# Performance work log

Measured on AMD Instinct MI355X. Metric: run time of the kernel, lower is better.

Reference implementation:

```python
import jax, jax.numpy as jnp
import numpy as np

N_NODES = 100000
N_EDGES = 1600000
F_IN = 512
HID = 128
N_CLASS = 6


def setup_inputs() -> dict:
    key = jax.random.key(0)
    ks = jax.random.split(key, 12)
    def unif(k, shape, stdv):
        return jax.random.uniform(k, shape, jnp.float32, -stdv, stdv)
    s1 = 1.0 / np.sqrt(HID); s4 = 1.0 / np.sqrt(N_CLASS)
    return {
        "x": jax.random.normal(ks[0], (N_NODES, F_IN), jnp.float32),
        "edge_row": jax.random.randint(ks[1], (N_EDGES,), 0, N_NODES, jnp.int32),
        "edge_col": jax.random.randint(ks[2], (N_EDGES,), 0, N_NODES, jnp.int32),
        "edge_weight": jax.random.uniform(ks[3], (N_EDGES,), jnp.float32),
        "W1": unif(ks[4], (F_IN, HID), s1), "b1": unif(ks[5], (HID,), s1),
        "W2": unif(ks[6], (HID, HID), s1), "b2": unif(ks[7], (HID,), s1),
        "W3": unif(ks[8], (HID, HID), s1), "b3": unif(ks[9], (HID,), s1),
        "W4": unif(ks[10], (HID, N_CLASS), s4), "b4": unif(ks[11], (N_CLASS,), s4),
    }


def _gcn_layer(x, row, col, w_e, W, b):
    # support = x @ W  (dense mm), then spmm(adj, support) in COO form:
    # out[i] = sum_{(i,j) in E} A[i,j] * support[j]
    support = x @ W                              # [N, F_out]
    msgs = support[col] * w_e[:, None]           # [E, F_out] gather + scale
    agg = jax.ops.segment_sum(msgs, row, num_segments=N_NODES)
    return agg + b


def reference(x, edge_row, edge_col, edge_weight, W1, b1, W2, b2, W3, b3, W4, b4):
    # eval mode: F.dropout(training=False) is identity
    h = jax.nn.relu(_gcn_layer(x, edge_row, edge_col, edge_weight, W1, b1))
    h = jax.nn.relu(_gcn_layer(h, edge_row, edge_col, edge_weight, W2, b2))
    h = jax.nn.relu(_gcn_layer(h, edge_row, edge_col, edge_weight, W3, b3))
    return _gcn_layer(h, edge_row, edge_col, edge_weight, W4, b4)
```

## Files before the change

### kernel.cpp

```cpp
#include <hip/hip_runtime.h>
#include <cstdint>

constexpr int NN = 100000;
constexpr int NE = 1600000;
constexpr int FIN = 512;
constexpr int HID = 128;
constexpr int NCLS = 6;
constexpr int EPAD = NE + 3 * NN;

typedef __attribute__((ext_vector_type(8))) short short8v;
typedef __attribute__((ext_vector_type(4))) float f32x4;

constexpr float WINV = 1.0f / 32767.0f;

__device__ __forceinline__ unsigned short f2bf(float f) {
    uint32_t u = __float_as_uint(f);
    uint32_t r = u + 0x7FFFu + ((u >> 16) & 1u);
    return (unsigned short)(r >> 16);
}
__device__ __forceinline__ float bflo(uint32_t u) { return __uint_as_float(u << 16); }
__device__ __forceinline__ float bfhi(uint32_t u) { return __uint_as_float(u & 0xffff0000u); }

__device__ __forceinline__ void gl_lds16(const void* g, void* l) {
    __builtin_amdgcn_global_load_lds(
        (const __attribute__((address_space(1))) unsigned int*)(unsigned long long)g,
        (__attribute__((address_space(3))) unsigned int*)(unsigned int)(unsigned long long)l,
        16, 0, 0);
}

__device__ __forceinline__ void cvt_body(const float* __restrict__ W,
                                         unsigned short* __restrict__ Bp, int t) {
    const int lane = t & 63;
    const int fi = t >> 6;
    const int n = fi & 7, ks = fi >> 3;
    const int krow = ks * 32 + (lane >> 4) * 8;
    const int col = n * 16 + (lane & 15);
    short8v sv;
    #pragma unroll
    for (int j = 0; j < 8; ++j) sv[j] = (short)f2bf(W[(size_t)(krow + j) * HID + col]);
    *(short8v*)&Bp[(size_t)t * 8] = sv;
}

__global__ void cvt_w3(const float* __restrict__ W1, const float* __restrict__ W2,
                       const float* __restrict__ W3,
                       unsigned short* __restrict__ Bp1, unsigned short* __restrict__ Bp2,
                       unsigned short* __restrict__ Bp3) {
    const int t = blockIdx.x * blockDim.x + threadIdx.x;
    constexpr int T1 = (FIN / 32) * 8 * 64;
    constexpr int T2 = (HID / 32) * 8 * 64;
    if (t < T1)                cvt_body(W1, Bp1, t);
    else if (t < T1 + T2)      cvt_body(W2, Bp2, t - T1);
    else if (t < T1 + 2 * T2)  cvt_body(W3, Bp3, t - T1 - T2);
}

template<int K, bool ABF>
__launch_bounds__(320)
__global__ void gemm_lds(const void* __restrict__ Av, const unsigned short* __restrict__ Bp,
                         unsigned short* __restrict__ C) {
    constexpr int BM    = 160;
    constexpr int KS    = 32;
    constexpr int EB    = ABF ? 2 : 4;
    constexpr int ROWB  = KS * EB;
    constexpr int SLOTS = ROWB / 16;
    constexpr int SMSK  = SLOTS - 1;
    constexpr int CHUNK = BM * ROWB;
    constexpr int WBYT  = CHUNK / 5;
    constexpr int NISS  = WBYT / 1024;
    constexpr int NS    = K / KS;

    __shared__ __attribute__((aligned(16))) unsigned char lds[2 * CHUNK];

    const int tid  = threadIdx.x;
    const int lane = tid & 63;
    const int wave = tid >> 6;
    const int row0 = blockIdx.x * BM;
    const int lr   = lane & 15;
    const int kg   = lane >> 4;

    const unsigned char* Ab = (const unsigned char*)Av;
    const size_t rowbytes = (size_t)K * EB;

    auto stage = [&](int bufsel, int ks) {
        const size_t kbyte = (size_t)ks * ROWB;
        #pragma unroll
        for (int i = 0; i < NISS; ++i) {
            const int Lw   = wave * WBYT + i * 1024 + lane * 16;
            const int row  = Lw / ROWB;
            const int slot = (Lw >> 4) & SMSK;
            const int src  = slot ^ (row & SMSK);
            const unsigned char* g = Ab + (size_t)(row0 + row) * rowbytes + kbyte + src * 16;
            void* l = (void*)&lds[bufsel * CHUNK + wave * WBYT + i * 1024];
            gl_lds16(g, l);
        }
    };

    f32x4 acc[2][8] = {};

    stage(0, 0);

    int cur = 0;
    for (int ks = 0; ks < NS; ++ks) {
        short8v bfr[8];
        const unsigned short* bb = Bp + ((size_t)ks * 8 * 64 + lane) * 8;
        #pragma unroll
        for (int n = 0; n < 8; ++n)
            bfr[n] = *reinterpret_cast<const short8v*>(bb + (size_t)n * 64 * 8);

        if (ks + 1 < NS) {
            stage(cur ^ 1, ks + 1);
            asm volatile("s_waitcnt vmcnt(%0)" :: "i"(NISS) : "memory");
        } else {
            asm volatile("s_waitcnt vmcnt(0)" ::: "memory");
        }
        __builtin_amdgcn_sched_barrier(0);

        const unsigned char* base = &lds[cur * CHUNK];
        const int rA0 = wave * 32 + lr;
        const int rA1 = rA0 + 16;
        const int key = lr & SMSK;

        short8v a0, a1;
        if constexpr (ABF) {
            a0 = *(const short8v*)(base + rA0 * ROWB + ((kg ^ key) * 16));
            a1 = *(const short8v*)(base + rA1 * ROWB + ((kg ^ key) * 16));
        } else {
            const float4 f00 = *(const float4*)(base + rA0 * ROWB + (((2 * kg + 0) ^ key) * 16));
            const float4 f01 = *(const float4*)(base + rA0 * ROWB + (((2 * kg + 1) ^ key) * 16));
            const float4 f10 = *(const float4*)(base + rA1 * ROWB + (((2 * kg + 0) ^ key) * 16));
            const float4 f11 = *(const float4*)(base + rA1 * ROWB + (((2 * kg + 1) ^ key) * 16));
            a0[0] = (short)f2bf(f00.x); a0[1] = (short)f2bf(f00.y);
            a0[2] = (short)f2bf(f00.z); a0[3] = (short)f2bf(f00.w);
            a0[4] = (short)f2bf(f01.x); a0[5] = (short)f2bf(f01.y);
            a0[6] = (short)f2bf(f01.z); a0[7] = (short)f2bf(f01.w);
            a1[0] = (short)f2bf(f10.x); a1[1] = (short)f2bf(f10.y);
            a1[2] = (short)f2bf(f10.z); a1[3] = (short)f2bf(f10.w);
            a1[4] = (short)f2bf(f11.x); a1[5] = (short)f2bf(f11.y);
            a1[6] = (short)f2bf(f11.z); a1[7] = (short)f2bf(f11.w);
        }

        #pragma unroll
        for (int n = 0; n < 8; ++n) {
            acc[0][n] = __builtin_amdgcn_mfma_f32_16x16x32_bf16(a0, bfr[n], acc[0][n], 0, 0, 0);
            acc[1][n] = __builtin_amdgcn_mfma_f32_16x16x32_bf16(a1, bfr[n], acc[1][n], 0, 0, 0);
        }
        cur ^= 1;
    }

    #pragma unroll
    for (int m = 0; m < 2; ++m)
        #pragma unroll
        for (int n = 0; n < 8; ++n)
            #pragma unroll
            for (int i = 0; i < 4; ++i) {
                const int r = row0 + wave * 32 + m * 16 + kg * 4 + i;
                C[(size_t)r * HID + n * 16 + lr] = f2bf(acc[m][n][i]);
            }
}

__global__ void gemm_w4(const unsigned short* __restrict__ H, const float* __restrict__ W,
                        float* __restrict__ S, int M) {
    __shared__ float Ws[HID * NCLS];
    for (int i = threadIdx.x; i < HID * NCLS; i += blockDim.x) Ws[i] = W[i];
    __syncthreads();
    const int r = blockIdx.x * blockDim.x + threadIdx.x;
    if (r >= M) return;
    float acc[NCLS] = {};
    const unsigned short* h = &H[(size_t)r * HID];
    for (int k0 = 0; k0 < HID; k0 += 8) {
        const uint4 hv = *reinterpret_cast<const uint4*>(&h[k0]);
        float hf[8];
        hf[0] = bflo(hv.x); hf[1] = bfhi(hv.x);
        hf[2] = bflo(hv.y); hf[3] = bfhi(hv.y);
        hf[4] = bflo(hv.z); hf[5] = bfhi(hv.z);
        hf[6] = bflo(hv.w); hf[7] = bfhi(hv.w);
        #pragma unroll
        for (int u = 0; u < 8; ++u)
            #pragma unroll
            for (int j = 0; j < NCLS; ++j)
                acc[j] = fmaf(hf[u], Ws[(k0 + u) * NCLS + j], acc[j]);
    }
    #pragma unroll
    for (int j = 0; j < NCLS; ++j) S[(size_t)r * NCLS + j] = acc[j];
}

__global__ void hist_k(const int* __restrict__ erow, int* __restrict__ cnt) {
    const int e = blockIdx.x * blockDim.x + threadIdx.x;
    if (e < NE) atomicAdd(&cnt[erow[e]], 1);
}

__global__ void scan1_k(const int* __restrict__ in, int* __restrict__ out,
                        int* __restrict__ bsum, int n) {
    __shared__ int s[256];
    const int tid = threadIdx.x;
    const int gid = blockIdx.x * 256 + tid;
    const int v = (gid < NN) ? ((in[gid] + 3) & ~3) : 0;
    s[tid] = v;
    __syncthreads();
    for (int off = 1; off < 256; off <<= 1) {
        const int t = (tid >= off) ? s[tid - off] : 0;
        __syncthreads();
        s[tid] += t;
        __syncthreads();
    }
    if (gid < n) out[gid] = s[tid] - v;
    if (tid == 255) bsum[blockIdx.x] = s[255];
}

__global__ void scan2_k(int* __restrict__ bsum, int nb) {
    __shared__ int s[512];
    const int tid = threadIdx.x;
    const int v = (tid < nb) ? bsum[tid] : 0;
    s[tid] = v;
    __syncthreads();
    for (int off = 1; off < 512; off <<= 1) {
        const int t = (tid >= off) ? s[tid - off] : 0;
        __syncthreads();
        s[tid] += t;
        __syncthreads();
    }
    if (tid < nb) bsum[tid] = s[tid] - v;
}

__global__ void scan3_k(int* __restrict__ out, const int* __restrict__ bsum, int n) {
    const int gid = blockIdx.x * 256 + threadIdx.x;
    if (gid < n) out[gid] += bsum[blockIdx.x];
}

__global__ void scatter_k(const int* __restrict__ erow, const int* __restrict__ ecol,
                          const float* __restrict__ ew,
                          const int* __restrict__ row_ptr, int* __restrict__ cur,
                          uint32_t* __restrict__ edges) {
    const int e = blockIdx.x * blockDim.x + threadIdx.x;
    if (e >= NE) return;
    const int r = erow[e];
    const int pos = row_ptr[r] + atomicAdd(&cur[r], 1);
    const uint32_t wq = (uint32_t)(ew[e] * 32767.0f + 0.5f);
    edges[pos] = ((uint32_t)ecol[e] << 15) | wq;
}

__global__ void pad_k(const int* __restrict__ row_ptr, const int* __restrict__ cur,
                      uint32_t* __restrict__ edges) {
    const int r = blockIdx.x * blockDim.x + threadIdx.x;
    if (r >= NN) return;
    const int end = row_ptr[r + 1];
    for (int p = row_ptr[r] + cur[r]; p < end; ++p) edges[p] = 0u;
}

template<bool RELU>
__launch_bounds__(256)
__global__ void spmm_bf16(const int* __restrict__ row_ptr,
                          const uint32_t* __restrict__ edges,
                          const unsigned short* __restrict__ S,
                          const float* __restrict__ bias,
                          unsigned short* __restrict__ out) {
    const int lane = threadIdx.x & 63;
    const int row = blockIdx.x * 4 + (threadIdx.x >> 6);
    if (row >= NN) return;
    const int beg = row_ptr[row];
    const int end = row_ptr[row + 1];
    const int fo = lane * 2;
    float2 a0 = *reinterpret_cast<const float2*>(&bias[fo]);
    float2 a1 = {0.f, 0.f}, a2 = {0.f, 0.f}, a3 = {0.f, 0.f};

    int j = beg;
    for (; j + 16 <= end; j += 16) {
        uint4 e0 = *reinterpret_cast<const uint4*>(edges + j);
        uint4 e1 = *reinterpret_cast<const uint4*>(edges + j + 4);
        uint4 e2 = *reinterpret_cast<const uint4*>(edges + j + 8);
        uint4 e3 = *reinterpret_cast<const uint4*>(edges + j + 12);
        const uint32_t ea[16] = {e0.x, e0.y, e0.z, e0.w, e1.x, e1.y, e1.z, e1.w,
                                 e2.x, e2.y, e2.z, e2.w, e3.x, e3.y, e3.z, e3.w};
        uint32_t s[16];
        #pragma unroll
        for (int q = 0; q < 16; ++q)
            s[q] = *reinterpret_cast<const uint32_t*>(&S[(size_t)(ea[q] >> 15) * HID + fo]);
        #pragma unroll
        for (int q = 0; q < 4; ++q) {
            const float w0 = (float)(ea[q]      & 0x7FFFu) * WINV;
            const float w1 = (float)(ea[q + 4]  & 0x7FFFu) * WINV;
            const float w2 = (float)(ea[q + 8]  & 0x7FFFu) * WINV;
            const float w3 = (float)(ea[q + 12] & 0x7FFFu) * WINV;
            a0.x = fmaf(bflo(s[q]),      w0, a0.x); a0.y = fmaf(bfhi(s[q]),      w0, a0.y);
            a1.x = fmaf(bflo(s[q + 4]),  w1, a1.x); a1.y = fmaf(bfhi(s[q + 4]),  w1, a1.y);
            a2.x = fmaf(bflo(s[q + 8]),  w2, a2.x); a2.y = fmaf(bfhi(s[q + 8]),  w2, a2.y);
            a3.x = fmaf(bflo(s[q + 12]), w3, a3.x); a3.y = fmaf(bfhi(s[q + 12]), w3, a3.y);
        }
    }
    for (; j < end; j += 4) {
        const uint4 e = *reinterpret_cast<const uint4*>(edges + j);
        const uint32_t ea[4] = {e.x, e.y, e.z, e.w};
        uint32_t s[4];
        #pragma unroll
        for (int q = 0; q < 4; ++q)
            s[q] = *reinterpret_cast<const uint32_t*>(&S[(size_t)(ea[q] >> 15) * HID + fo]);
        const float w0 = (float)(ea[0] & 0x7FFFu) * WINV;
        const float w1 = (float)(ea[1] & 0x7FFFu) * WINV;
        const float w2 = (float)(ea[2] & 0x7FFFu) * WINV;
        const float w3 = (float)(ea[3] & 0x7FFFu) * WINV;
        a0.x = fmaf(bflo(s[0]), w0, a0.x); a0.y = fmaf(bfhi(s[0]), w0, a0.y);
        a1.x = fmaf(bflo(s[1]), w1, a1.x); a1.y = fmaf(bfhi(s[1]), w1, a1.y);
        a2.x = fmaf(bflo(s[2]), w2, a2.x); a2.y = fmaf(bfhi(s[2]), w2, a2.y);
        a3.x = fmaf(bflo(s[3]), w3, a3.x); a3.y = fmaf(bfhi(s[3]), w3, a3.y);
    }
    float fx = (a0.x + a1.x) + (a2.x + a3.x);
    float fy = (a0.y + a1.y) + (a2.y + a3.y);
    if (RELU) { fx = fmaxf(fx, 0.f); fy = fmaxf(fy, 0.f); }
    const uint32_t o = (uint32_t)f2bf(fx) | ((uint32_t)f2bf(fy) << 16);
    *reinterpret_cast<uint32_t*>(&out[(size_t)row * HID + fo]) = o;
}

__launch_bounds__(256)
__global__ void spmm6(const int* __restrict__ row_ptr,
                      const uint32_t* __restrict__ edges,
                      const float* __restrict__ S,
                      const float* __restrict__ bias,
                      float* __restrict__ out) {
    const int t = blockIdx.x * blockDim.x + threadIdx.x;
    const int row = t >> 4;
    const int sl = t & 15;
    if (row >= NN) return;
    const int beg = row_ptr[row];
    const int end = row_ptr[row + 1];
    float acc[NCLS] = {};
    for (int j = beg + sl; j < end; j += 16) {
        const uint32_t e = edges[j];
        const float w = (float)(e & 0x7FFFu) * WINV;
        const float* s = &S[(size_t)(e >> 15) * NCLS];
        #pragma unroll
        for (int k = 0; k < NCLS; ++k) acc[k] = fmaf(s[k], w, acc[k]);
    }
    #pragma unroll
    for (int off = 8; off > 0; off >>= 1)
        #pragma unroll
        for (int k = 0; k < NCLS; ++k) acc[k] += __shfl_xor(acc[k], off, 64);
    if (sl == 0) {
        #pragma unroll
        for (int k = 0; k < NCLS; ++k) out[(size_t)row * NCLS + k] = acc[k] + bias[k];
    }
}

extern "C" void kernel_launch(void* const* d_in, const int* in_sizes, int n_in,
                              void* d_out, int out_size, void* d_ws, size_t ws_size,
                              hipStream_t stream) {
    const float* x    = (const float*)d_in[0];
    const int*   erow = (const int*)d_in[1];
    const int*   ecol = (const int*)d_in[2];
    const float* ew   = (const float*)d_in[3];
    const float* W1 = (const float*)d_in[4];  const float* b1 = (const float*)d_in[5];
    const float* W2 = (const float*)d_in[6];  const float* b2 = (const float*)d_in[7];
    const float* W3 = (const float*)d_in[8];  const float* b3 = (const float*)d_in[9];
    const float* W4 = (const float*)d_in[10]; const float* b4 = (const float*)d_in[11];
    float* out = (float*)d_out;

    uint32_t*       edges_s = (uint32_t*)d_ws;
    unsigned short* sup16   = (unsigned short*)(edges_s + EPAD);
    unsigned short* h16     = sup16 + (size_t)NN * HID;
    float*          sup6    = (float*)(h16 + (size_t)NN * HID);
    unsigned short* Bp1     = (unsigned short*)(sup6 + (size_t)NN * NCLS);
    unsigned short* Bp2     = Bp1 + (size_t)FIN * HID;
    unsigned short* Bp3     = Bp2 + (size_t)HID * HID;
    int*            row_ptr = (int*)(Bp3 + (size_t)HID * HID);
    int*            row_cnt = row_ptr + (NN + 1);
    int*            row_cur = row_cnt + NN;
    int*            bsum    = row_cur + NN;

    const dim3 blk(256);
    const int  g_edge = (NE + 255) / 256;
    const int  NB = (NN + 1 + 255) / 256;

    cvt_w3<<<(12288 + 255) / 256, blk, 0, stream>>>(W1, W2, W3, Bp1, Bp2, Bp3);

    hipMemsetAsync(row_cnt, 0, (size_t)2 * NN * sizeof(int), stream);
    hist_k<<<g_edge, blk, 0, stream>>>(erow, row_cnt);
    scan1_k<<<NB, blk, 0, stream>>>(row_cnt, row_ptr, bsum, NN + 1);
    scan2_k<<<1, 512, 0, stream>>>(bsum, NB);
    scan3_k<<<NB, blk, 0, stream>>>(row_ptr, bsum, NN + 1);
    scatter_k<<<g_edge, blk, 0, stream>>>(erow, ecol, ew, row_ptr, row_cur, edges_s);
    pad_k<<<(NN + 255) / 256, blk, 0, stream>>>(row_ptr, row_cur, edges_s);

    const int g_gemm = NN / 160;
    const int g_spmm = NN / 4;

    gemm_lds<FIN, false><<<g_gemm, dim3(320), 0, stream>>>(x, Bp1, sup16);
    spmm_bf16<true><<<g_spmm, blk, 0, stream>>>(row_ptr, edges_s, sup16, b1, h16);
    gemm_lds<HID, true><<<g_gemm, dim3(320), 0, stream>>>(h16, Bp2, sup16);
    spmm_bf16<true><<<g_spmm, blk, 0, stream>>>(row_ptr, edges_s, sup16, b2, h16);
    gemm_lds<HID, true><<<g_gemm, dim3(320), 0, stream>>>(h16, Bp3, sup16);
    spmm_bf16<true><<<g_spmm, blk, 0, stream>>>(row_ptr, edges_s, sup16, b3, h16);
    gemm_w4<<<(NN + 255) / 256, blk, 0, stream>>>(h16, W4, sup6, NN);
    spmm6<<<(NN * 16 + 255) / 256, blk, 0, stream>>>(row_ptr, edges_s, sup6, b4, out);
}
```

Measured before the change: 449.6 us.

## Make bf16 SpMM persistent with software-prefetched row pointers and edges

```diff
diff --git a/kernel.cpp b/kernel.cpp
--- a/kernel.cpp
+++ b/kernel.cpp
@@ -252,61 +252,95 @@
                           const uint32_t* __restrict__ edges,
                           const unsigned short* __restrict__ S,
                           const float* __restrict__ bias,
-                          unsigned short* __restrict__ out) {
+                          unsigned short* __restrict__ out,
+                          int nwv) {
     const int lane = threadIdx.x & 63;
-    const int row = blockIdx.x * 4 + (threadIdx.x >> 6);
+    int row = (blockIdx.x * blockDim.x + threadIdx.x) >> 6;
     if (row >= NN) return;
-    const int beg = row_ptr[row];
-    const int end = row_ptr[row + 1];
     const int fo = lane * 2;
-    float2 a0 = *reinterpret_cast<const float2*>(&bias[fo]);
-    float2 a1 = {0.f, 0.f}, a2 = {0.f, 0.f}, a3 = {0.f, 0.f};
-
-    int j = beg;
-    for (; j + 16 <= end; j += 16) {
-        uint4 e0 = *reinterpret_cast<const uint4*>(edges + j);
-        uint4 e1 = *reinterpret_cast<const uint4*>(edges + j + 4);
-        uint4 e2 = *reinterpret_cast<const uint4*>(edges + j + 8);
-        uint4 e3 = *reinterpret_cast<const uint4*>(edges + j + 12);
-        const uint32_t ea[16] = {e0.x, e0.y, e0.z, e0.w, e1.x, e1.y, e1.z, e1.w,
-                                 e2.x, e2.y, e2.z, e2.w, e3.x, e3.y, e3.z, e3.w};
+    const float2 bv = *reinterpret_cast<const float2*>(&bias[fo]);
+
+    int beg = row_ptr[row];
+    int end = row_ptr[row + 1];
+    uint4 c0 = *reinterpret_cast<const uint4*>(edges + beg);
+    uint4 c1 = *reinterpret_cast<const uint4*>(edges + beg + 4);
+    uint4 c2 = *reinterpret_cast<const uint4*>(edges + beg + 8);
+    uint4 c3 = *reinterpret_cast<const uint4*>(edges + beg + 12);
+    int nrow = row + nwv;
+    int nbeg = 0, nend = 0;
+    if (nrow < NN) { nbeg = row_ptr[nrow]; nend = row_ptr[nrow + 1]; }
+
+    while (true) {
+        uint32_t ea[16] = {c0.x, c0.y, c0.z, c0.w, c1.x, c1.y, c1.z, c1.w,
+                           c2.x, c2.y, c2.z, c2.w, c3.x, c3.y, c3.z, c3.w};
         uint32_t s[16];
         #pragma unroll
         for (int q = 0; q < 16; ++q)
             s[q] = *reinterpret_cast<const uint32_t*>(&S[(size_t)(ea[q] >> 15) * HID + fo]);
-        #pragma unroll
-        for (int q = 0; q < 4; ++q) {
-            const float w0 = (float)(ea[q]      & 0x7FFFu) * WINV;
-            const float w1 = (float)(ea[q + 4]  & 0x7FFFu) * WINV;
-            const float w2 = (float)(ea[q + 8]  & 0x7FFFu) * WINV;
-            const float w3 = (float)(ea[q + 12] & 0x7FFFu) * WINV;
-            a0.x = fmaf(bflo(s[q]),      w0, a0.x); a0.y = fmaf(bfhi(s[q]),      w0, a0.y);
-            a1.x = fmaf(bflo(s[q + 4]),  w1, a1.x); a1.y = fmaf(bfhi(s[q + 4]),  w1, a1.y);
-            a2.x = fmaf(bflo(s[q + 8]),  w2, a2.x); a2.y = fmaf(bfhi(s[q + 8]),  w2, a2.y);
-            a3.x = fmaf(bflo(s[q + 12]), w3, a3.x); a3.y = fmaf(bfhi(s[q + 12]), w3, a3.y);
-        }
-    }
-    for (; j < end; j += 4) {
-        const uint4 e = *reinterpret_cast<const uint4*>(edges + j);
-        const uint32_t ea[4] = {e.x, e.y, e.z, e.w};
-        uint32_t s[4];
-        #pragma unroll
-        for (int q = 0; q < 4; ++q)
-            s[q] = *reinterpret_cast<const uint32_t*>(&S[(size_t)(ea[q] >> 15) * HID + fo]);
-        const float w0 = (float)(ea[0] & 0x7FFFu) * WINV;
-        const float w1 = (float)(ea[1] & 0x7FFFu) * WINV;
-        const float w2 = (float)(ea[2] & 0x7FFFu) * WINV;
-        const float w3 = (float)(ea[3] & 0x7FFFu) * WINV;
-        a0.x = fmaf(bflo(s[0]), w0, a0.x); a0.y = fmaf(bfhi(s[0]), w0, a0.y);
-        a1.x = fmaf(bflo(s[1]), w1, a1.x); a1.y = fmaf(bfhi(s[1]), w1, a1.y);
-        a2.x = fmaf(bflo(s[2]), w2, a2.x); a2.y = fmaf(bfhi(s[2]), w2, a2.y);
-        a3.x = fmaf(bflo(s[3]), w3, a3.x); a3.y = fmaf(bfhi(s[3]), w3, a3.y);
-    }
-    float fx = (a0.x + a1.x) + (a2.x + a3.x);
-    float fy = (a0.y + a1.y) + (a2.y + a3.y);
-    if (RELU) { fx = fmaxf(fx, 0.f); fy = fmaxf(fy, 0.f); }
-    const uint32_t o = (uint32_t)f2bf(fx) | ((uint32_t)f2bf(fy) << 16);
-    *reinterpret_cast<uint32_t*>(&out[(size_t)row * HID + fo]) = o;
+
+        uint4 n0, n1, n2, n3;
+        if (nrow < NN) {
+            n0 = *reinterpret_cast<const uint4*>(edges + nbeg);
+            n1 = *reinterpret_cast<const uint4*>(edges + nbeg + 4);
+            n2 = *reinterpret_cast<const uint4*>(edges + nbeg + 8);
+            n3 = *reinterpret_cast<const uint4*>(edges + nbeg + 12);
+        }
+        const int nnrow = nrow + nwv;
+        int nnbeg = 0, nnend = 0;
+        if (nnrow < NN) { nnbeg = row_ptr[nnrow]; nnend = row_ptr[nnrow + 1]; }
+
+        float2 a0 = bv, a1 = {0.f, 0.f}, a2 = {0.f, 0.f}, a3 = {0.f, 0.f};
+        if (beg < end) {
+            const float w0 = (float)(ea[0] & 0x7FFFu) * WINV;
+            const float w1 = (float)(ea[1] & 0x7FFFu) * WINV;
+            const float w2 = (float)(ea[2] & 0x7FFFu) * WINV;
+            const float w3 = (float)(ea[3] & 0x7FFFu) * WINV;
+            a0.x = fmaf(bflo(s[0]), w0, a0.x); a0.y = fmaf(bfhi(s[0]), w0, a0.y);
+            a1.x = fmaf(bflo(s[1]), w1, a1.x); a1.y = fmaf(bfhi(s[1]), w1, a1.y);
+            a2.x = fmaf(bflo(s[2]), w2, a2.x); a2.y = fmaf(bfhi(s[2]), w2, a2.y);
+            a3.x = fmaf(bflo(s[3]), w3, a3.x); a3.y = fmaf(bfhi(s[3]), w3, a3.y);
+        }
+        #pragma unroll
+        for (int g = 1; g < 4; ++g) {
+            if (beg + 4 * g < end) {
+                const float w0 = (float)(ea[4*g]     & 0x7FFFu) * WINV;
+                const float w1 = (float)(ea[4*g + 1] & 0x7FFFu) * WINV;
+                const float w2 = (float)(ea[4*g + 2] & 0x7FFFu) * WINV;
+                const float w3 = (float)(ea[4*g + 3] & 0x7FFFu) * WINV;
+                a0.x = fmaf(bflo(s[4*g]),     w0, a0.x); a0.y = fmaf(bfhi(s[4*g]),     w0, a0.y);
+                a1.x = fmaf(bflo(s[4*g + 1]), w1, a1.x); a1.y = fmaf(bfhi(s[4*g + 1]), w1, a1.y);
+                a2.x = fmaf(bflo(s[4*g + 2]), w2, a2.x); a2.y = fmaf(bfhi(s[4*g + 2]), w2, a2.y);
+                a3.x = fmaf(bflo(s[4*g + 3]), w3, a3.x); a3.y = fmaf(bfhi(s[4*g + 3]), w3, a3.y);
+            }
+        }
+        for (int j = beg + 16; j < end; j += 4) {
+            const uint4 e = *reinterpret_cast<const uint4*>(edges + j);
+            const uint32_t eb[4] = {e.x, e.y, e.z, e.w};
+            uint32_t t[4];
+            #pragma unroll
+            for (int q = 0; q < 4; ++q)
+                t[q] = *reinterpret_cast<const uint32_t*>(&S[(size_t)(eb[q] >> 15) * HID + fo]);
+            const float w0 = (float)(eb[0] & 0x7FFFu) * WINV;
+            const float w1 = (float)(eb[1] & 0x7FFFu) * WINV;
+            const float w2 = (float)(eb[2] & 0x7FFFu) * WINV;
+            const float w3 = (float)(eb[3] & 0x7FFFu) * WINV;
+            a0.x = fmaf(bflo(t[0]), w0, a0.x); a0.y = fmaf(bfhi(t[0]), w0, a0.y);
+            a1.x = fmaf(bflo(t[1]), w1, a1.x); a1.y = fmaf(bfhi(t[1]), w1, a1.y);
+            a2.x = fmaf(bflo(t[2]), w2, a2.x); a2.y = fmaf(bfhi(t[2]), w2, a2.y);
+            a3.x = fmaf(bflo(t[3]), w3, a3.x); a3.y = fmaf(bfhi(t[3]), w3, a3.y);
+        }
+
+        float fx = (a0.x + a1.x) + (a2.x + a3.x);
+        float fy = (a0.y + a1.y) + (a2.y + a3.y);
+        if (RELU) { fx = fmaxf(fx, 0.f); fy = fmaxf(fy, 0.f); }
+        const uint32_t o = (uint32_t)f2bf(fx) | ((uint32_t)f2bf(fy) << 16);
+        *reinterpret_cast<uint32_t*>(&out[(size_t)row * HID + fo]) = o;
+
+        if (nrow >= NN) break;
+        row = nrow; beg = nbeg; end = nend;
+        c0 = n0; c1 = n1; c2 = n2; c3 = n3;
+        nrow = nnrow; nbeg = nnbeg; nend = nnend;
+    }
 }
 
 __launch_bounds__(256)
@@ -379,14 +413,15 @@
     pad_k<<<(NN + 255) / 256, blk, 0, stream>>>(row_ptr, row_cur, edges_s);
 
     const int g_gemm = NN / 160;
-    const int g_spmm = NN / 4;
+    const int g_spmm = 1536;
+    const int nwv    = g_spmm * 4;
 
     gemm_lds<FIN, false><<<g_gemm, dim3(320), 0, stream>>>(x, Bp1, sup16);
-    spmm_bf16<true><<<g_spmm, blk, 0, stream>>>(row_ptr, edges_s, sup16, b1, h16);
+    spmm_bf16<true><<<g_spmm, blk, 0, stream>>>(row_ptr, edges_s, sup16, b1, h16, nwv);
     gemm_lds<HID, true><<<g_gemm, dim3(320), 0, stream>>>(h16, Bp2, sup16);
-    spmm_bf16<true><<<g_spmm, blk, 0, stream>>>(row_ptr, edges_s, sup16, b2, h16);
+    spmm_bf16<true><<<g_spmm, blk, 0, stream>>>(row_ptr, edges_s, sup16, b2, h16, nwv);
     gemm_lds<HID, true><<<g_gemm, dim3(320), 0, stream>>>(h16, Bp3, sup16);
-    spmm_bf16<true><<<g_spmm, blk, 0, stream>>>(row_ptr, edges_s, sup16, b3, h16);
+    spmm_bf16<true><<<g_spmm, blk, 0, stream>>>(row_ptr, edges_s, sup16, b3, h16, nwv);
     gemm_w4<<<(NN + 255) / 256, blk, 0, stream>>>(h16, W4, sup6, NN);
     spmm6<<<(NN * 16 + 255) / 256, blk, 0, stream>>>(row_ptr, edges_s, sup6, b4, out);
 }
```

After: 467.3 us. 3.9% more time.

## Split support matrix into 64-column halves and vectorize edge-preprocessing kernels

Applied to the files above, without the earlier changes.

```diff
diff --git a/kernel.cpp b/kernel.cpp
--- a/kernel.cpp
+++ b/kernel.cpp
@@ -56,7 +56,7 @@
 template<int K, bool ABF>
 __launch_bounds__(320)
 __global__ void gemm_lds(const void* __restrict__ Av, const unsigned short* __restrict__ Bp,
-                         unsigned short* __restrict__ C) {
+                         unsigned short* __restrict__ Sc) {
     constexpr int BM    = 160;
     constexpr int KS    = 32;
     constexpr int EB    = ABF ? 2 : 4;
@@ -153,7 +153,7 @@
             #pragma unroll
             for (int i = 0; i < 4; ++i) {
                 const int r = row0 + wave * 32 + m * 16 + kg * 4 + i;
-                C[(size_t)r * HID + n * 16 + lr] = f2bf(acc[m][n][i]);
+                Sc[((size_t)(n >> 2) * NN + r) * 64 + (n & 3) * 16 + lr] = f2bf(acc[m][n][i]);
             }
 }
 
@@ -183,9 +183,14 @@
     for (int j = 0; j < NCLS; ++j) S[(size_t)r * NCLS + j] = acc[j];
 }
 
-__global__ void hist_k(const int* __restrict__ erow, int* __restrict__ cnt) {
-    const int e = blockIdx.x * blockDim.x + threadIdx.x;
-    if (e < NE) atomicAdd(&cnt[erow[e]], 1);
+__global__ void hist_k(const int4* __restrict__ erow4, int* __restrict__ cnt) {
+    const int t = blockIdx.x * blockDim.x + threadIdx.x;
+    if (t >= NE / 4) return;
+    const int4 r = erow4[t];
+    atomicAdd(&cnt[r.x], 1);
+    atomicAdd(&cnt[r.y], 1);
+    atomicAdd(&cnt[r.z], 1);
+    atomicAdd(&cnt[r.w], 1);
 }
 
 __global__ void scan1_k(const int* __restrict__ in, int* __restrict__ out,
@@ -226,16 +231,31 @@
     if (gid < n) out[gid] += bsum[blockIdx.x];
 }
 
-__global__ void scatter_k(const int* __restrict__ erow, const int* __restrict__ ecol,
-                          const float* __restrict__ ew,
+__global__ void scatter_k(const int4* __restrict__ erow4, const int4* __restrict__ ecol4,
+                          const float4* __restrict__ ew4,
                           const int* __restrict__ row_ptr, int* __restrict__ cur,
                           uint32_t* __restrict__ edges) {
-    const int e = blockIdx.x * blockDim.x + threadIdx.x;
-    if (e >= NE) return;
-    const int r = erow[e];
-    const int pos = row_ptr[r] + atomicAdd(&cur[r], 1);
-    const uint32_t wq = (uint32_t)(ew[e] * 32767.0f + 0.5f);
-    edges[pos] = ((uint32_t)ecol[e] << 15) | wq;
+    const int t = blockIdx.x * blockDim.x + threadIdx.x;
+    if (t >= NE / 4) return;
+    const int4 r = erow4[t];
+    const int4 c = ecol4[t];
+    const float4 w = ew4[t];
+    {
+        const int pos = row_ptr[r.x] + atomicAdd(&cur[r.x], 1);
+        edges[pos] = ((uint32_t)c.x << 15) | (uint32_t)(w.x * 32767.0f + 0.5f);
+    }
+    {
+        const int pos = row_ptr[r.y] + atomicAdd(&cur[r.y], 1);
+        edges[pos] = ((uint32_t)c.y << 15) | (uint32_t)(w.y * 32767.0f + 0.5f);
+    }
+    {
+        const int pos = row_ptr[r.z] + atomicAdd(&cur[r.z], 1);
+        edges[pos] = ((uint32_t)c.z << 15) | (uint32_t)(w.z * 32767.0f + 0.5f);
+    }
+    {
+        const int pos = row_ptr[r.w] + atomicAdd(&cur[r.w], 1);
+        edges[pos] = ((uint32_t)c.w << 15) | (uint32_t)(w.w * 32767.0f + 0.5f);
+    }
 }
 
 __global__ void pad_k(const int* __restrict__ row_ptr, const int* __restrict__ cur,
@@ -248,19 +268,21 @@
 
 template<bool RELU>
 __launch_bounds__(256)
-__global__ void spmm_bf16(const int* __restrict__ row_ptr,
+__global__ void spmm_half(const int* __restrict__ row_ptr,
                           const uint32_t* __restrict__ edges,
-                          const unsigned short* __restrict__ S,
+                          const unsigned short* __restrict__ Sc,
                           const float* __restrict__ bias,
                           unsigned short* __restrict__ out) {
     const int lane = threadIdx.x & 63;
-    const int row = blockIdx.x * 4 + (threadIdx.x >> 6);
+    const int half = blockIdx.x & 1;
+    const int row = (blockIdx.x >> 1) * 4 + (threadIdx.x >> 6);
     if (row >= NN) return;
     const int beg = row_ptr[row];
     const int end = row_ptr[row + 1];
-    const int fo = lane * 2;
-    float2 a0 = *reinterpret_cast<const float2*>(&bias[fo]);
-    float2 a1 = {0.f, 0.f}, a2 = {0.f, 0.f}, a3 = {0.f, 0.f};
+    const unsigned short* S = Sc + (size_t)half * NN * 64 + lane;
+
+    float a0 = bias[half * 64 + lane];
+    float a1 = 0.f, a2 = 0.f, a3 = 0.f;
 
     int j = beg;
     for (; j + 16 <= end; j += 16) {
@@ -273,17 +295,19 @@
         uint32_t s[16];
         #pragma unroll
         for (int q = 0; q < 16; ++q)
-            s[q] = *reinterpret_cast<const uint32_t*>(&S[(size_t)(ea[q] >> 15) * HID + fo]);
+            s[q] = (uint32_t)S[(size_t)(ea[q] >> 15) * 64];
         #pragma unroll
         for (int q = 0; q < 4; ++q) {
             const float w0 = (float)(ea[q]      & 0x7FFFu) * WINV;
             const float w1 = (float)(ea[q + 4]  & 0x7FFFu) * WINV;
             const float w2 = (float)(ea[q + 8]  & 0x7FFFu) * WINV;
             const float w3 = (float)(ea[q + 12] & 0x7FFFu) * WINV;
-            a0.x = fmaf(bflo(s[q]),      w0, a0.x); a0.y = fmaf(bfhi(s[q]),      w0, a0.y);
-            a1.x = fmaf(bflo(s[q + 4]),  w1, a1.x); a1.y = fmaf(bfhi(s[q + 4]),  w1, a1.y);
-            a2.x = fmaf(bflo(s[q + 8]),  w2, a2.x); a2.y = fmaf(bfhi(s[q + 8]),  w2, a2.y);
-            a3.x = fmaf(bflo(s[q + 12]), w3, a3.x); a3.y = fmaf(bfhi(s[q + 12]), w3, a3.y);
+            a0 = fmaf(bflo(s[q] << 16),      w0 * 65536.f, a0 * 1.f),
+            a0 = a0;
+            a0 = fmaf(bflo(s[q]),      w0, a0);
+            a1 = fmaf(bflo(s[q + 4]),  w1, a1);
+            a2 = fmaf(bflo(s[q + 8]),  w2, a2);
+            a3 = fmaf(bflo(s[q + 12]), w3, a3);
         }
     }
     for (; j < end; j += 4) {
@@ -292,21 +316,15 @@
         uint32_t s[4];
         #pragma unroll
         for (int q = 0; q < 4; ++q)
-            s[q] = *reinterpret_cast<const uint32_t*>(&S[(size_t)(ea[q] >> 15) * HID + fo]);
-        const float w0 = (float)(ea[0] & 0x7FFFu) * WINV;
-        const float w1 = (float)(ea[1] & 0x7FFFu) * WINV;
-        const float w2 = (float)(ea[2] & 0x7FFFu) * WINV;
-        const float w3 = (float)(ea[3] & 0x7FFFu) * WINV;
-        a0.x = fmaf(bflo(s[0]), w0, a0.x); a0.y = fmaf(bfhi(s[0]), w0, a0.y);
-        a1.x = fmaf(bflo(s[1]), w1, a1.x); a1.y = fmaf(bfhi(s[1]), w1, a1.y);
-        a2.x = fmaf(bflo(s[2]), w2, a2.x); a2.y = fmaf(bfhi(s[2]), w2, a2.y);
-        a3.x = fmaf(bflo(s[3]), w3, a3.x); a3.y = fmaf(bfhi(s[3]), w3, a3.y);
-    }
-    float fx = (a0.x + a1.x) + (a2.x + a3.x);
-    float fy = (a0.y + a1.y) + (a2.y + a3.y);
-    if (RELU) { fx = fmaxf(fx, 0.f); fy = fmaxf(fy, 0.f); }
-    const uint32_t o = (uint32_t)f2bf(fx) | ((uint32_t)f2bf(fy) << 16);
-    *reinterpret_cast<uint32_t*>(&out[(size_t)row * HID + fo]) = o;
+            s[q] = (uint32_t)S[(size_t)(ea[q] >> 15) * 64];
+        a0 = fmaf(bflo(s[0]), (float)(ea[0] & 0x7FFFu) * WINV, a0);
+        a1 = fmaf(bflo(s[1]), (float)(ea[1] & 0x7FFFu) * WINV, a1);
+        a2 = fmaf(bflo(s[2]), (float)(ea[2] & 0x7FFFu) * WINV, a2);
+        a3 = fmaf(bflo(s[3]), (float)(ea[3] & 0x7FFFu) * WINV, a3);
+    }
+    float f = (a0 + a1) + (a2 + a3);
+    if (RELU) f = fmaxf(f, 0.f);
+    out[(size_t)row * HID + half * 64 + lane] = f2bf(f);
 }
 
 __launch_bounds__(256)
@@ -365,28 +383,29 @@
     int*            bsum    = row_cur + NN;
 
     const dim3 blk(256);
-    const int  g_edge = (NE + 255) / 256;
+    const int  g_edge4 = (NE / 4 + 255) / 256;
     const int  NB = (NN + 1 + 255) / 256;
 
     cvt_w3<<<(12288 + 255) / 256, blk, 0, stream>>>(W1, W2, W3, Bp1, Bp2, Bp3);
 
     hipMemsetAsync(row_cnt, 0, (size_t)2 * NN * sizeof(int), stream);
-    hist_k<<<g_edge, blk, 0, stream>>>(erow, row_cnt);
+    hist_k<<<g_edge4, blk, 0, stream>>>((const int4*)erow, row_cnt);
     scan1_k<<<NB, blk, 0, stream>>>(row_cnt, row_ptr, bsum, NN + 1);
     scan2_k<<<1, 512, 0, stream>>>(bsum, NB);
     scan3_k<<<NB, blk, 0, stream>>>(row_ptr, bsum, NN + 1);
-    scatter_k<<<g_edge, blk, 0, stream>>>(erow, ecol, ew, row_ptr, row_cur, edges_s);
+    scatter_k<<<g_edge4, blk, 0, stream>>>((const int4*)erow, (const int4*)ecol,
+                                           (const float4*)ew, row_ptr, row_cur, edges_s);
     pad_k<<<(NN + 255) / 256, blk, 0, stream>>>(row_ptr, row_cur, edges_s);
 
     const int g_gemm = NN / 160;
-    const int g_spmm = NN / 4;
+    const int g_spmm = 2 * ((NN + 3) / 4);
 
     gemm_lds<FIN, false><<<g_gemm, dim3(320), 0, stream>>>(x, Bp1, sup16);
-    spmm_bf16<true><<<g_spmm, blk, 0, stream>>>(row_ptr, edges_s, sup16, b1, h16);
+    spmm_half<true><<<g_spmm, blk, 0, stream>>>(row_ptr, edges_s, sup16, b1, h16);
     gemm_lds<HID, true><<<g_gemm, dim3(320), 0, stream>>>(h16, Bp2, sup16);
-    spmm_bf16<true><<<g_spmm, blk, 0, stream>>>(row_ptr, edges_s, sup16, b2, h16);
+    spmm_half<true><<<g_spmm, blk, 0, stream>>>(row_ptr, edges_s, sup16, b2, h16);
     gemm_lds<HID, true><<<g_gemm, dim3(320), 0, stream>>>(h16, Bp3, sup16);
-    spmm_bf16<true><<<g_spmm, blk, 0, stream>>>(row_ptr, edges_s, sup16, b3, h16);
+    spmm_half<true><<<g_spmm, blk, 0, stream>>>(row_ptr, edges_s, sup16, b3, h16);
     gemm_w4<<<(NN + 255) / 256, blk, 0, stream>>>(h16, W4, sup6, NN);
     spmm6<<<(NN * 16 + 255) / 256, blk, 0, stream>>>(row_ptr, edges_s, sup6, b4, out);
 }
```

Result: slower. 509.9 us (+13.4%).

## Horizontally fuse histogram with weight conversion and layer-1 GEMM with edge scatter

Applied to the files above, without the earlier changes.

```diff
diff --git a/kernel.cpp b/kernel.cpp
--- a/kernel.cpp
+++ b/kernel.cpp
@@ -41,22 +41,11 @@
     *(short8v*)&Bp[(size_t)t * 8] = sv;
 }
 
-__global__ void cvt_w3(const float* __restrict__ W1, const float* __restrict__ W2,
-                       const float* __restrict__ W3,
-                       unsigned short* __restrict__ Bp1, unsigned short* __restrict__ Bp2,
-                       unsigned short* __restrict__ Bp3) {
-    const int t = blockIdx.x * blockDim.x + threadIdx.x;
-    constexpr int T1 = (FIN / 32) * 8 * 64;
-    constexpr int T2 = (HID / 32) * 8 * 64;
-    if (t < T1)                cvt_body(W1, Bp1, t);
-    else if (t < T1 + T2)      cvt_body(W2, Bp2, t - T1);
-    else if (t < T1 + 2 * T2)  cvt_body(W3, Bp3, t - T1 - T2);
-}
-
 template<int K, bool ABF>
-__launch_bounds__(320)
-__global__ void gemm_lds(const void* __restrict__ Av, const unsigned short* __restrict__ Bp,
-                         unsigned short* __restrict__ C) {
+__device__ __forceinline__ void gemm_body(unsigned char* lds,
+                                          const void* __restrict__ Av,
+                                          const unsigned short* __restrict__ Bp,
+                                          unsigned short* __restrict__ C, int bid) {
     constexpr int BM    = 160;
     constexpr int KS    = 32;
     constexpr int EB    = ABF ? 2 : 4;
@@ -68,12 +57,10 @@
     constexpr int NISS  = WBYT / 1024;
     constexpr int NS    = K / KS;
 
-    __shared__ __attribute__((aligned(16))) unsigned char lds[2 * CHUNK];
-
     const int tid  = threadIdx.x;
     const int lane = tid & 63;
     const int wave = tid >> 6;
-    const int row0 = blockIdx.x * BM;
+    const int row0 = bid * BM;
     const int lr   = lane & 15;
     const int kg   = lane >> 4;
 
@@ -157,6 +144,82 @@
             }
 }
 
+__launch_bounds__(320)
+__global__ void gemm_lds_bf(const void* __restrict__ Av, const unsigned short* __restrict__ Bp,
+                            unsigned short* __restrict__ C) {
+    __shared__ __attribute__((aligned(16))) unsigned char lds[2 * 160 * 64];
+    gemm_body<HID, true>(lds, Av, Bp, C, blockIdx.x);
+}
+
+__device__ __forceinline__ void scatter_one(int r, int c, float w,
+                                            const int* __restrict__ row_ptr,
+                                            int* __restrict__ cur,
+                                            uint32_t* __restrict__ edges) {
+    const int pos = row_ptr[r] + atomicAdd(&cur[r], 1);
+    edges[pos] = ((uint32_t)c << 15) | (uint32_t)(w * 32767.0f + 0.5f);
+}
+
+__global__ void fused_hist_cvt(const int4* __restrict__ erow4, int* __restrict__ cnt,
+                               const float* __restrict__ W1, const float* __restrict__ W2,
+                               const float* __restrict__ W3,
+                               unsigned short* __restrict__ Bp1, unsigned short* __restrict__ Bp2,
+                               unsigned short* __restrict__ Bp3) {
+    constexpr int NB_HIST = (NE / 4 + 255) / 256;
+    const int bid = blockIdx.x;
+    if (bid < NB_HIST) {
+        const int t = bid * 256 + threadIdx.x;
+        if (t < NE / 4) {
+            const int4 r = erow4[t];
+            atomicAdd(&cnt[r.x], 1);
+            atomicAdd(&cnt[r.y], 1);
+            atomicAdd(&cnt[r.z], 1);
+            atomicAdd(&cnt[r.w], 1);
+        }
+    } else {
+        const int t = (bid - NB_HIST) * 256 + threadIdx.x;
+        constexpr int T1 = (FIN / 32) * 8 * 64;
+        constexpr int T2 = (HID / 32) * 8 * 64;
+        if (t < T1)                cvt_body(W1, Bp1, t);
+        else if (t < T1 + T2)      cvt_body(W2, Bp2, t - T1);
+        else if (t < T1 + 2 * T2)  cvt_body(W3, Bp3, t - T1 - T2);
+    }
+}
+
+constexpr int GB_GEMM = NN / 160;
+constexpr int GB_SCAT = (NE / 4 + 319) / 320;
+constexpr int GB_PAD  = (NN + 319) / 320;
+
+__launch_bounds__(320)
+__global__ void fused_l1(const float* __restrict__ x, const unsigned short* __restrict__ Bp1,
+                         unsigned short* __restrict__ sup16,
+                         const int4* __restrict__ erow4, const int4* __restrict__ ecol4,
+                         const float4* __restrict__ ew4,
+                         const int* __restrict__ row_ptr, const int* __restrict__ row_cnt,
+                         int* __restrict__ cur, uint32_t* __restrict__ edges) {
+    __shared__ __attribute__((aligned(16))) unsigned char lds[2 * 160 * 128];
+    const int bid = blockIdx.x;
+    if (bid < GB_GEMM) {
+        gemm_body<FIN, false>(lds, x, Bp1, sup16, bid);
+    } else if (bid < GB_GEMM + GB_SCAT) {
+        const int t = (bid - GB_GEMM) * 320 + threadIdx.x;
+        if (t < NE / 4) {
+            const int4 r = erow4[t];
+            const int4 c = ecol4[t];
+            const float4 w = ew4[t];
+            scatter_one(r.x, c.x, w.x, row_ptr, cur, edges);
+            scatter_one(r.y, c.y, w.y, row_ptr, cur, edges);
+            scatter_one(r.z, c.z, w.z, row_ptr, cur, edges);
+            scatter_one(r.w, c.w, w.w, row_ptr, cur, edges);
+        }
+    } else {
+        const int r = (bid - GB_GEMM - GB_SCAT) * 320 + threadIdx.x;
+        if (r < NN) {
+            const int end = row_ptr[r + 1];
+            for (int p = row_ptr[r] + row_cnt[r]; p < end; ++p) edges[p] = 0u;
+        }
+    }
+}
+
 __global__ void gemm_w4(const unsigned short* __restrict__ H, const float* __restrict__ W,
                         float* __restrict__ S, int M) {
     __shared__ float Ws[HID * NCLS];
@@ -183,11 +246,6 @@
     for (int j = 0; j < NCLS; ++j) S[(size_t)r * NCLS + j] = acc[j];
 }
 
-__global__ void hist_k(const int* __restrict__ erow, int* __restrict__ cnt) {
-    const int e = blockIdx.x * blockDim.x + threadIdx.x;
-    if (e < NE) atomicAdd(&cnt[erow[e]], 1);
-}
-
 __global__ void scan1_k(const int* __restrict__ in, int* __restrict__ out,
                         int* __restrict__ bsum, int n) {
     __shared__ int s[256];
@@ -224,26 +282,6 @@
 __global__ void scan3_k(int* __restrict__ out, const int* __restrict__ bsum, int n) {
     const int gid = blockIdx.x * 256 + threadIdx.x;
     if (gid < n) out[gid] += bsum[blockIdx.x];
-}
-
-__global__ void scatter_k(const int* __restrict__ erow, const int* __restrict__ ecol,
-                          const float* __restrict__ ew,
-                          const int* __restrict__ row_ptr, int* __restrict__ cur,
-                          uint32_t* __restrict__ edges) {
-    const int e = blockIdx.x * blockDim.x + threadIdx.x;
-    if (e >= NE) return;
-    const int r = erow[e];
-    const int pos = row_ptr[r] + atomicAdd(&cur[r], 1);
-    const uint32_t wq = (uint32_t)(ew[e] * 32767.0f + 0.5f);
-    edges[pos] = ((uint32_t)ecol[e] << 15) | wq;
-}
-
-__global__ void pad_k(const int* __restrict__ row_ptr, const int* __restrict__ cur,
-                      uint32_t* __restrict__ edges) {
-    const int r = blockIdx.x * blockDim.x + threadIdx.x;
-    if (r >= NN) return;
-    const int end = row_ptr[r + 1];
-    for (int p = row_ptr[r] + cur[r]; p < end; ++p) edges[p] = 0u;
 }
 
 template<bool RELU>
@@ -365,27 +403,27 @@
     int*            bsum    = row_cur + NN;
 
     const dim3 blk(256);
-    const int  g_edge = (NE + 255) / 256;
     const int  NB = (NN + 1 + 255) / 256;
-
-    cvt_w3<<<(12288 + 255) / 256, blk, 0, stream>>>(W1, W2, W3, Bp1, Bp2, Bp3);
+    constexpr int NB_HIST = (NE / 4 + 255) / 256;
+    constexpr int NB_CVT  = 12288 / 256;
 
     hipMemsetAsync(row_cnt, 0, (size_t)2 * NN * sizeof(int), stream);
-    hist_k<<<g_edge, blk, 0, stream>>>(erow, row_cnt);
+    fused_hist_cvt<<<NB_HIST + NB_CVT, blk, 0, stream>>>(
+        (const int4*)erow, row_cnt, W1, W2, W3, Bp1, Bp2, Bp3);
+
     scan1_k<<<NB, blk, 0, stream>>>(row_cnt, row_ptr, bsum, NN + 1);
     scan2_k<<<1, 512, 0, stream>>>(bsum, NB);
     scan3_k<<<NB, blk, 0, stream>>>(row_ptr, bsum, NN + 1);
-    scatter_k<<<g_edge, blk, 0, stream>>>(erow, ecol, ew, row_ptr, row_cur, edges_s);
-    pad_k<<<(NN + 255) / 256, blk, 0, stream>>>(row_ptr, row_cur, edges_s);
-
-    const int g_gemm = NN / 160;
+
+    fused_l1<<<GB_GEMM + GB_SCAT + GB_PAD, dim3(320), 0, stream>>>(
+        x, Bp1, sup16, (const int4*)erow, (const int4*)ecol, (const float4*)ew,
+        row_ptr, row_cnt, row_cur, edges_s);
+
     const int g_spmm = NN / 4;
-
-    gemm_lds<FIN, false><<<g_gemm, dim3(320), 0, stream>>>(x, Bp1, sup16);
     spmm_bf16<true><<<g_spmm, blk, 0, stream>>>(row_ptr, edges_s, sup16, b1, h16);
-    gemm_lds<HID, true><<<g_gemm, dim3(320), 0, stream>>>(h16, Bp2, sup16);
+    gemm_lds_bf<<<GB_GEMM, dim3(320), 0, stream>>>(h16, Bp2, sup16);
     spmm_bf16<true><<<g_spmm, blk, 0, stream>>>(row_ptr, edges_s, sup16, b2, h16);
-    gemm_lds<HID, true><<<g_gemm, dim3(320), 0, stream>>>(h16, Bp3, sup16);
+    gemm_lds_bf<<<GB_GEMM, dim3(320), 0, stream>>>(h16, Bp3, sup16);
     spmm_bf16<true><<<g_spmm, blk, 0, stream>>>(row_ptr, edges_s, sup16, b3, h16);
     gemm_w4<<<(NN + 255) / 256, blk, 0, stream>>>(h16, W4, sup6, NN);
     spmm6<<<(NN * 16 + 255) / 256, blk, 0, stream>>>(row_ptr, edges_s, sup6, b4, out);
```

New measurement: 418.5 us. 6.9% less time.
